# Kernel optimization log

Hardware: AMD Instinct MI355X
Metric: run time of the kernel (lower is better)

Reference implementation:

```python
import jax, jax.numpy as jnp
import numpy as np

TAU = 2.0
V_TH = 0.5
BN_EPS = 1e-5
ALPHA = 2.0  # spikingjelly surrogate.ATan default

@jax.custom_vjp
def spike_fn(x):
    # Heaviside forward, ATan surrogate backward (defined for fwdbwd parity)
    return (x >= 0.0).astype(x.dtype)

def _spike_fwd(x):
    return spike_fn(x), x

def _spike_bwd(x, g):
    return (g * (ALPHA / 2.0) / (1.0 + (jnp.pi / 2.0 * ALPHA * x) ** 2),)

spike_fn.defvjp(_spike_fwd, _spike_bwd)

def lif_multistep(x_seq):
    # MultiStepLIFNode: v <- v + (x - v)/tau ; spike = H(v - v_th) ; hard reset v<-v*(1-sg(spike))
    def step(v, x_t):
        v = v + (x_t - v) / TAU
        s = spike_fn(v - V_TH)
        v = v * (1.0 - jax.lax.stop_gradient(s))  # detach_reset=True, v_reset=0
        return v, s
    v0 = jnp.zeros_like(x_seq[0])
    _, spikes = jax.lax.scan(step, v0, x_seq)
    return spikes

def setup_inputs() -> dict:
    key = jax.random.key(0)
    k1, k2, k3 = jax.random.split(key, 3)
    T, B, N, D = 4, 64, 256, 512
    x = jax.random.normal(k1, (T, B, N, D), jnp.float32)
    mx = jax.random.normal(k2, (N, B, T, D), jnp.float32)
    W = jax.random.normal(k3, (D, D), jnp.float32) / np.sqrt(D).astype(np.float32)
    gamma = jnp.ones((D,), jnp.float32)
    beta = jnp.zeros((D,), jnp.float32)
    return {"x": x, "mx": mx, "W": W, "gamma": gamma, "beta": beta}

def reference(x, mx, W, gamma, beta):
    # mx: [N,B,T,D] -> transpose(0,2) -> [T,B,N,D]
    mxt = jnp.transpose(mx, (2, 1, 0, 3))
    # Linear (no bias): [T,B,N,D] @ W^T
    h = jnp.einsum('tbnd,ed->tbne', mxt, W)
    # BatchNorm1d(D) in training mode: stats over (T*B, N) per channel D (biased var)
    mean = h.mean(axis=(0, 1, 2))
    var = h.var(axis=(0, 1, 2))
    hn = (h - mean) * jax.lax.rsqrt(var + BN_EPS) * gamma + beta
    # LIF recurrence over T
    s = lif_multistep(hn)  # [T,B,N,D] binary spikes
    return x * s
```

## Files before the change

kernel.cpp:

```cpp
#include <hip/hip_runtime.h>
#include <math.h>

namespace {
constexpr int TDIM = 4, BDIM = 64, NDIM = 256, DDIM = 512;
constexpr int MROWS = 65536;
constexpr long long BND = 8388608LL;
constexpr double BN_EPS = 1e-5;

constexpr int BM = 64, BNT = 128, BK = 32;
constexpr int APITCH = BK + 2;
constexpr int WPITCH = BNT + 4;
constexpr int LDS_BYTES = (BM * APITCH + BK * WPITCH) * 8;

constexpr int BM3 = 128, BN3 = 64, BK3 = 16;
constexpr int AP3 = BM3 + 1;
constexpr int WP3 = BN3 + 1;

constexpr int NSA = 6, NSW = 5;
constexpr long long APL = 33554432LL;
constexpr long long WPL = 262144LL;
constexpr int LDSA8 = NSA * 64 * 64;
constexpr int LDSW8 = NSW * 64 * 64;
}

typedef double d4 __attribute__((ext_vector_type(4)));
typedef int i32x4 __attribute__((ext_vector_type(4)));
typedef int i32x16 __attribute__((ext_vector_type(16)));

__global__ void probe_k(double* __restrict__ rowmap)
{
    const int l = threadIdx.x;
    d4 z = {0.0, 0.0, 0.0, 0.0};
    d4 dr = __builtin_amdgcn_mfma_f64_16x16x4f64((double)(l & 15), 1.0, z, 0, 0, 0);
#pragma unroll
    for (int r = 0; r < 4; ++r)
        rowmap[l * 4 + r] = dr[r] * 0.25;
}

__global__ void probe8_k(double* __restrict__ irow8, double* __restrict__ icol8)
{
    const int l = threadIdx.x;
    i32x16 z;
#pragma unroll
    for (int r = 0; r < 16; ++r) z[r] = 0;
    const int mb = (l & 31) * 0x01010101;
    const int ob = 0x01010101;
    i32x4 am = {mb, mb, mb, mb};
    i32x4 a1 = {ob, ob, ob, ob};
    i32x16 d1 = __builtin_amdgcn_mfma_i32_32x32x32_i8(am, a1, z, 0, 0, 0);
#pragma unroll
    for (int r = 0; r < 16; ++r)
        irow8[l * 16 + r] = (double)d1[r] / 32.0;
    i32x16 d2 = __builtin_amdgcn_mfma_i32_32x32x32_i8(a1, am, z, 0, 0, 0);
    icol8[l] = (double)d2[0] / 32.0;
}

template<int NS>
__global__ __launch_bounds__(256)
void slice_k(const float* __restrict__ src, char* __restrict__ dst,
             long long n, long long plane, double F)
{
    const long long base = ((long long)blockIdx.x * 256 + threadIdx.x) * 8;
    if (base >= n) return;
    const float4 v0 = *(const float4*)(src + base);
    const float4 v1 = *(const float4*)(src + base + 4);
    const float vv[8] = {v0.x, v0.y, v0.z, v0.w, v1.x, v1.y, v1.z, v1.w};
    unsigned long long pk[NS];
#pragma unroll
    for (int s = 0; s < NS; ++s) pk[s] = 0ULL;
#pragma unroll
    for (int e = 0; e < 8; ++e) {
        double V = (double)vv[e] * F;
        double u = rint(V);
        double r = V - u;
        pk[0] |= ((unsigned long long)(unsigned char)(signed char)(int)u) << (8 * e);
#pragma unroll
        for (int s = 1; s < NS; ++s) {
            r *= 128.0;
            u = rint(r);
            r -= u;
            pk[s] |= ((unsigned long long)(unsigned char)(signed char)(int)u) << (8 * e);
        }
    }
#pragma unroll
    for (int s = 0; s < NS; ++s)
        *(unsigned long long*)(dst + s * plane + base) = pk[s];
}

__global__ __launch_bounds__(256, 2)
void gemm8_k(const char* __restrict__ Asl, const char* __restrict__ Wsl,
             double* __restrict__ hbuf, double* __restrict__ sums,
             const double* __restrict__ irow8, const double* __restrict__ icol8)
{
    __shared__ __align__(16) char sm8[LDSA8 + LDSW8];

    const int tid = threadIdx.x;
    const int bid = blockIdx.x;
    const int rb  = ((bid >> 6) << 3) | (bid & 7);
    const int cb  = (bid >> 3) & 7;
    const int row0 = rb * 64;
    const int col0 = cb * 64;

    const int w  = tid >> 6;
    const int l  = tid & 63;
    const int wr = w >> 1;
    const int wc = w & 1;

    const int sr = tid >> 2;
    const int sk = (tid & 3) * 16;
    const long long aoff = (long long)(row0 + sr) * DDIM + sk;
    const long long woff = (long long)(col0 + sr) * DDIM + sk;

    i32x16 acc[7];
#pragma unroll
    for (int g = 0; g < 7; ++g)
#pragma unroll
        for (int r = 0; r < 16; ++r) acc[g][r] = 0;

    i32x4 pfa[NSA], pfw[NSW];
#pragma unroll
    for (int s = 0; s < NSA; ++s)
        pfa[s] = *(const i32x4*)(Asl + s * APL + aoff);
#pragma unroll
    for (int s = 0; s < NSW; ++s)
        pfw[s] = *(const i32x4*)(Wsl + s * WPL + woff);

    const int swzS = (sr & 7) << 4;
    const int swzL = (l & 7) << 4;

    for (int c = 0; c < 8; ++c) {
        __syncthreads();
#pragma unroll
        for (int s = 0; s < NSA; ++s)
            *(i32x4*)(sm8 + ((s * 4096 + sr * 64 + sk) ^ swzS)) = pfa[s];
#pragma unroll
        for (int s = 0; s < NSW; ++s)
            *(i32x4*)(sm8 + LDSA8 + ((s * 4096 + sr * 64 + sk) ^ swzS)) = pfw[s];
        __syncthreads();

        if (c < 7) {
#pragma unroll
            for (int s = 0; s < NSA; ++s)
                pfa[s] = *(const i32x4*)(Asl + s * APL + aoff + (c + 1) * 64);
#pragma unroll
            for (int s = 0; s < NSW; ++s)
                pfw[s] = *(const i32x4*)(Wsl + s * WPL + woff + (c + 1) * 64);
        }

        const int arowB = (32 * wr + (l & 31)) * 64 + ((l >> 5) * 16);
        const int wrowB = (32 * wc + (l & 31)) * 64 + ((l >> 5) * 16);
#pragma unroll
        for (int h = 0; h < 2; ++h) {
            i32x4 af[NSA], wf[NSW];
#pragma unroll
            for (int s = 0; s < NSA; ++s)
                af[s] = *(const i32x4*)(sm8 + ((s * 4096 + arowB + h * 32) ^ swzL));
#pragma unroll
            for (int s = 0; s < NSW; ++s)
                wf[s] = *(const i32x4*)(sm8 + LDSA8 + ((s * 4096 + wrowB + h * 32) ^ swzL));
#pragma unroll
            for (int s = 0; s < NSA; ++s)
#pragma unroll
                for (int t = 0; t < NSW; ++t)
                    if (s + t <= 6)
                        acc[s + t] = __builtin_amdgcn_mfma_i32_32x32x32_i8(
                                         af[s], wf[t], acc[s + t], 0, 0, 0);
        }
    }

    int irw[16];
#pragma unroll
    for (int r = 0; r < 16; ++r) irw[r] = (int)irow8[l * 16 + r];
    const int icl = (int)icol8[l];

    const double C7 = 1.0 / 128.0, CMB = 1.0 / 1024.0;
    double lsum = 0.0, lsq = 0.0;
    const int colg = col0 + 32 * wc + icl;
#pragma unroll
    for (int r = 0; r < 16; ++r) {
        double t = (double)acc[6][r];
        t = fma(t, C7, (double)acc[5][r]);
        t = fma(t, C7, (double)acc[4][r]);
        t = fma(t, C7, (double)acc[3][r]);
        t = fma(t, C7, (double)acc[2][r]);
        t = fma(t, C7, (double)acc[1][r]);
        t = fma(t, C7, (double)acc[0][r]);
        const double h = t * CMB;
        const int rowg = row0 + 32 * wr + irw[r];
        hbuf[(size_t)rowg * DDIM + colg] = h;
        lsum += h;
        lsq = fma(h, h, lsq);
    }

    __syncthreads();
    double* Ss = (double*)sm8;
    const int ctr = wr * 2 + (l >> 5);
    const int cloc = 32 * wc + icl;
    Ss[cloc * 4 + ctr] = lsum;
    Ss[256 + cloc * 4 + ctr] = lsq;
    __syncthreads();
    if (tid < 64) {
        double s = 0.0, q = 0.0;
#pragma unroll
        for (int k = 0; k < 4; ++k) {
            s += Ss[tid * 4 + k];
            q += Ss[256 + tid * 4 + k];
        }
        atomicAdd(&sums[col0 + tid], s);
        atomicAdd(&sums[512 + col0 + tid], q);
    }
}

__global__ __launch_bounds__(256, 2)
void gemm3_k(const float* __restrict__ mx, const float* __restrict__ Wm,
             double* __restrict__ hbuf, double* __restrict__ sums,
             const double* __restrict__ rowmap)
{
    __shared__ double Atr[BK3 * AP3];
    __shared__ double Wt [BK3 * WP3];

    const int tid = threadIdx.x;
    const int bid = blockIdx.x;
    const int rb  = ((bid >> 6) << 3) | (bid & 7);
    const int cb  = (bid >> 3) & 7;
    const int row0 = rb * BM3;
    const int col0 = cb * BN3;

    const int w  = tid >> 6;
    const int l  = tid & 63;
    const int wr = w >> 1;
    const int wc = w & 1;
    const int lr = l & 15;
    const int kq = l >> 4;

    int irow[4];
#pragma unroll
    for (int r = 0; r < 4; ++r)
        irow[r] = (int)rowmap[l * 4 + r];

    const int arow = tid >> 1;
    const int af   = (tid & 1) * 8;
    const int wrow = tid >> 2;
    const int wf   = (tid & 3) * 4;
    const float* aSrc = mx + (size_t)(row0 + arow) * DDIM + af;
    const float* wSrc = Wm + (size_t)(col0 + wrow) * DDIM + wf;

    d4 acc[4][2];
#pragma unroll
    for (int i = 0; i < 4; ++i)
#pragma unroll
        for (int j = 0; j < 2; ++j) acc[i][j] = (d4){0.0, 0.0, 0.0, 0.0};

    float4 pa0 = *(const float4*)(aSrc + 0);
    float4 pa1 = *(const float4*)(aSrc + 4);
    float4 pw  = *(const float4*)(wSrc + 0);

    for (int kk = 0; kk < DDIM; kk += BK3) {
        __syncthreads();
        Atr[(af + 0) * AP3 + arow] = (double)pa0.x;
        Atr[(af + 1) * AP3 + arow] = (double)pa0.y;
        Atr[(af + 2) * AP3 + arow] = (double)pa0.z;
        Atr[(af + 3) * AP3 + arow] = (double)pa0.w;
        Atr[(af + 4) * AP3 + arow] = (double)pa1.x;
        Atr[(af + 5) * AP3 + arow] = (double)pa1.y;
        Atr[(af + 6) * AP3 + arow] = (double)pa1.z;
        Atr[(af + 7) * AP3 + arow] = (double)pa1.w;
        Wt[(wf + 0) * WP3 + wrow] = (double)pw.x;
        Wt[(wf + 1) * WP3 + wrow] = (double)pw.y;
        Wt[(wf + 2) * WP3 + wrow] = (double)pw.z;
        Wt[(wf + 3) * WP3 + wrow] = (double)pw.w;
        __syncthreads();

        if (kk + BK3 < DDIM) {
            pa0 = *(const float4*)(aSrc + kk + BK3 + 0);
            pa1 = *(const float4*)(aSrc + kk + BK3 + 4);
            pw  = *(const float4*)(wSrc + kk + BK3 + 0);
        }

#pragma unroll
        for (int ks = 0; ks < BK3 / 4; ++ks) {
            const int kabs = ks * 4 + kq;
            double a[4], b[2];
#pragma unroll
            for (int i = 0; i < 4; ++i)
                a[i] = Atr[kabs * AP3 + 64 * wr + 16 * i + lr];
#pragma unroll
            for (int j = 0; j < 2; ++j)
                b[j] = Wt[kabs * WP3 + 32 * wc + 16 * j + lr];
#pragma unroll
            for (int i = 0; i < 4; ++i)
#pragma unroll
                for (int j = 0; j < 2; ++j)
                    acc[i][j] = __builtin_amdgcn_mfma_f64_16x16x4f64(
                                    a[i], b[j], acc[i][j], 0, 0, 0);
        }
    }

#pragma unroll
    for (int i = 0; i < 4; ++i) {
#pragma unroll
        for (int j = 0; j < 2; ++j) {
            const size_t cbase = (size_t)col0 + 32 * wc + 16 * j + lr;
            const size_t rbase = (size_t)row0 + 64 * wr + 16 * i;
#pragma unroll
            for (int r = 0; r < 4; ++r)
                hbuf[(rbase + irow[r]) * DDIM + cbase] = acc[i][j][r];
        }
    }

    __syncthreads();
    double* Ssum = Atr;
    double* Ssq  = Atr + 512;
    const int ctr = wr * 4 + kq;
#pragma unroll
    for (int j = 0; j < 2; ++j) {
        const int cloc = 32 * wc + 16 * j + lr;
        double s = 0.0, q = 0.0;
#pragma unroll
        for (int i = 0; i < 4; ++i)
#pragma unroll
            for (int r = 0; r < 4; ++r) {
                const double v = acc[i][j][r];
                s += v;
                q = fma(v, v, q);
            }
        Ssum[cloc * 8 + ctr] = s;
        Ssq [cloc * 8 + ctr] = q;
    }
    __syncthreads();
    if (tid < 64) {
        double s = 0.0, q = 0.0;
#pragma unroll
        for (int c = 0; c < 8; ++c) {
            s += Ssum[tid * 8 + c];
            q += Ssq [tid * 8 + c];
        }
        atomicAdd(&sums[col0 + tid], s);
        atomicAdd(&sums[512 + col0 + tid], q);
    }
}

template<int MODE>
__global__ __launch_bounds__(256)
void gemm_k(const float* __restrict__ mx, const float* __restrict__ Wm,
            double* __restrict__ hbuf, double* __restrict__ sums,
            const double* __restrict__ scale, const double* __restrict__ shiftv,
            const float* __restrict__ x, float* __restrict__ out)
{
    __shared__ __align__(16) char smem[LDS_BYTES];
    double (*Ald)[APITCH] = reinterpret_cast<double(*)[APITCH]>(smem);
    double (*Wld)[WPITCH] = reinterpret_cast<double(*)[WPITCH]>(smem + (size_t)BM * APITCH * 8);

    const int tid  = threadIdx.x;
    const int rb   = blockIdx.x >> 2;
    const int cb   = blockIdx.x & 3;
    const int row0 = rb * BM;
    const int col0 = cb * BNT;

    const int arow = tid >> 2;
    const int ak   = (tid & 3) * 8;
    const int erow = tid >> 1;
    const int wk   = (tid & 1) * 16;

    const float* aSrc = mx + (size_t)(row0 + arow) * DDIM;
    const float* wSrc = Wm + (size_t)(col0 + erow) * DDIM;

    const int rg = tid >> 4;
    const int cg = tid & 15;

    double acc[4][8];
#pragma unroll
    for (int i = 0; i < 4; ++i)
#pragma unroll
        for (int j = 0; j < 8; ++j) acc[i][j] = 0.0;

    for (int kk = 0; kk < DDIM; kk += BK) {
        const float4 a0 = *(const float4*)(aSrc + kk + ak);
        const float4 a1 = *(const float4*)(aSrc + kk + ak + 4);
        const float4 w0 = *(const float4*)(wSrc + kk + wk);
        const float4 w1 = *(const float4*)(wSrc + kk + wk + 4);
        const float4 w2 = *(const float4*)(wSrc + kk + wk + 8);
        const float4 w3 = *(const float4*)(wSrc + kk + wk + 12);
        __syncthreads();
        Ald[arow][ak + 0] = (double)a0.x; Ald[arow][ak + 1] = (double)a0.y;
        Ald[arow][ak + 2] = (double)a0.z; Ald[arow][ak + 3] = (double)a0.w;
        Ald[arow][ak + 4] = (double)a1.x; Ald[arow][ak + 5] = (double)a1.y;
        Ald[arow][ak + 6] = (double)a1.z; Ald[arow][ak + 7] = (double)a1.w;
        const float wfv[16] = {w0.x, w0.y, w0.z, w0.w, w1.x, w1.y, w1.z, w1.w,
                               w2.x, w2.y, w2.z, w2.w, w3.x, w3.y, w3.z, w3.w};
#pragma unroll
        for (int q = 0; q < 16; ++q) Wld[wk + q][erow] = (double)wfv[q];
        __syncthreads();

#pragma unroll 4
        for (int d = 0; d < BK; ++d) {
            double a[4], wv[8];
#pragma unroll
            for (int i = 0; i < 4; ++i) a[i] = Ald[rg * 4 + i][d];
#pragma unroll
            for (int j = 0; j < 8; ++j) wv[j] = Wld[d][cg * 8 + j];
#pragma unroll
            for (int i = 0; i < 4; ++i)
#pragma unroll
                for (int j = 0; j < 8; ++j)
                    acc[i][j] = fma(a[i], wv[j], acc[i][j]);
        }
    }

    if (MODE <= 1) {
        __syncthreads();
        double* scr = reinterpret_cast<double*>(smem);
#pragma unroll
        for (int j = 0; j < 8; ++j) {
            const double s = acc[0][j] + acc[1][j] + acc[2][j] + acc[3][j];
            const double q = acc[0][j]*acc[0][j] + acc[1][j]*acc[1][j]
                           + acc[2][j]*acc[2][j] + acc[3][j]*acc[3][j];
            scr[(cg * 8 + j) * 16 + rg] = s;
            scr[2048 + (cg * 8 + j) * 16 + rg] = q;
        }
        __syncthreads();
        if (tid < 128) {
            double s = 0.0, q = 0.0;
#pragma unroll
            for (int r = 0; r < 16; ++r) {
                s += scr[tid * 16 + r];
                q += scr[2048 + tid * 16 + r];
            }
            atomicAdd(&sums[col0 + tid], s);
            atomicAdd(&sums[512 + col0 + tid], q);
        }
    }

    if (MODE == 2) {
        const int p  = rb * 16 + rg;
        const int nn = p >> 6;
        const int bb = p & 63;
#pragma unroll
        for (int j = 0; j < 8; ++j) {
            const int e = col0 + cg * 8 + j;
            const double sc = scale[e];
            const double sh = shiftv[e];
            const size_t basex = (size_t)bb * (NDIM * DDIM) + (size_t)nn * DDIM + e;
            double v = 0.0;
#pragma unroll
            for (int t = 0; t < 4; ++t) {
                const double hn = fma(acc[t][j], sc, sh);
                v = v + (hn - v) / 2.0;
                const bool s = (v - 0.5) >= 0.0;
                const size_t xi = (size_t)t * BND + basex;
                out[xi] = s ? x[xi] : 0.0f;
                if (s) v = 0.0;
            }
        }
    }
}

__global__ void zero_k(double* sums)
{
    const int i = blockIdx.x * 256 + threadIdx.x;
    if (i < 1024) sums[i] = 0.0;
}

__global__ void stat_k(const double* __restrict__ sums,
                       const float* __restrict__ gamma, const float* __restrict__ beta,
                       double* __restrict__ scale, double* __restrict__ shiftv)
{
    const int e = blockIdx.x * 256 + threadIdx.x;
    if (e < 512) {
        const double mean = sums[e] * (1.0 / 65536.0);
        const double msq  = sums[512 + e] * (1.0 / 65536.0);
        const double var  = msq - mean * mean;
        const double inv  = 1.0 / sqrt(var + BN_EPS);
        const double g    = (double)gamma[e] * inv;
        scale[e]  = g;
        shiftv[e] = (double)beta[e] - mean * g;
    }
}

__global__ __launch_bounds__(256)
void lifh_k(const double* __restrict__ hbuf, const double* __restrict__ scale,
            const double* __restrict__ shiftv, const float* __restrict__ x,
            float* __restrict__ out)
{
    const size_t i = (size_t)blockIdx.x * 256 + threadIdx.x;
    const int e  = (int)(i & 511);
    const size_t p = i >> 9;
    const int nn = (int)(p >> 6);
    const int bb = (int)(p & 63);
    const double sc = scale[e];
    const double sh = shiftv[e];
    const double* hp = hbuf + p * 2048 + e;
    const size_t basex = (size_t)bb * (NDIM * DDIM) + (size_t)nn * DDIM + e;
    double v = 0.0;
#pragma unroll
    for (int t = 0; t < 4; ++t) {
        const double hn = fma(hp[(size_t)t * 512], sc, sh);
        v = v + (hn - v) / 2.0;
        const bool s = (v - 0.5) >= 0.0;
        const size_t xi = (size_t)t * BND + basex;
        out[xi] = s ? x[xi] : 0.0f;
        if (s) v = 0.0;
    }
}

extern "C" void kernel_launch(void* const* d_in, const int* in_sizes, int n_in,
                              void* d_out, int out_size, void* d_ws, size_t ws_size,
                              hipStream_t stream)
{
    const float* x     = (const float*)d_in[0];
    const float* mx    = (const float*)d_in[1];
    const float* Wm    = (const float*)d_in[2];
    const float* gamma = (const float*)d_in[3];
    const float* beta  = (const float*)d_in[4];
    float* out = (float*)d_out;

    char* ws = (char*)d_ws;
    double* sums   = (double*)ws;
    double* scale  = (double*)(ws + 8192);
    double* shiftv = scale + 512;
    double* rowmap = (double*)(ws + 16384);
    double* irow8  = (double*)(ws + 18432);
    double* icol8  = (double*)(ws + 26624);
    double* hbuf   = (double*)(ws + 32768);

    const size_t HBSZ   = (size_t)MROWS * DDIM * 8;
    const size_t OFF_AS = 32768 + HBSZ;
    const size_t ASSZ   = (size_t)NSA * APL;
    const size_t OFF_WS = OFF_AS + ASSZ;
    const size_t WSSZ   = (size_t)NSW * WPL;
    const size_t need8  = OFF_WS + WSSZ;
    const size_t need_h = 32768 + HBSZ;

    hipLaunchKernelGGL(zero_k, dim3(4), dim3(256), 0, stream, sums);

    if (ws_size >= need8) {
        char* Asl = ws + OFF_AS;
        char* Wsl = ws + OFF_WS;
        hipLaunchKernelGGL(probe8_k, dim3(1), dim3(64), 0, stream, irow8, icol8);
        hipLaunchKernelGGL((slice_k<NSA>), dim3(16384), dim3(256), 0, stream,
                           mx, Asl, APL, APL, 4.0);
        hipLaunchKernelGGL((slice_k<NSW>), dim3(128), dim3(256), 0, stream,
                           Wm, Wsl, WPL, WPL, 256.0);
        hipLaunchKernelGGL(gemm8_k, dim3(8192), dim3(256), 0, stream,
                           Asl, Wsl, hbuf, sums, irow8, icol8);
        hipLaunchKernelGGL(stat_k, dim3(2), dim3(256), 0, stream,
                           sums, gamma, beta, scale, shiftv);
        hipLaunchKernelGGL(lifh_k, dim3(32768), dim3(256), 0, stream,
                           hbuf, scale, shiftv, x, out);
    } else if (ws_size >= need_h) {
        hipLaunchKernelGGL(probe_k, dim3(1), dim3(64), 0, stream, rowmap);
        hipLaunchKernelGGL(gemm3_k, dim3(4096), dim3(256), 0, stream,
                           mx, Wm, hbuf, sums, rowmap);
        hipLaunchKernelGGL(stat_k, dim3(2), dim3(256), 0, stream,
                           sums, gamma, beta, scale, shiftv);
        hipLaunchKernelGGL(lifh_k, dim3(32768), dim3(256), 0, stream,
                           hbuf, scale, shiftv, x, out);
    } else {
        hipLaunchKernelGGL((gemm_k<0>), dim3(4096), dim3(256), 0, stream,
                           mx, Wm, nullptr, sums, nullptr, nullptr, nullptr, nullptr);
        hipLaunchKernelGGL(stat_k, dim3(2), dim3(256), 0, stream,
                           sums, gamma, beta, scale, shiftv);
        hipLaunchKernelGGL((gemm_k<2>), dim3(4096), dim3(256), 0, stream,
                           mx, Wm, nullptr, nullptr, scale, shiftv, x, out);
    }
}
```

Measured before the change: 557.5 us.

## Tile-major int8 slice layout with direct global-to-LDS double-buffered loads

```diff
diff --git a/kernel.cpp b/kernel.cpp
--- a/kernel.cpp
+++ b/kernel.cpp
@@ -19,13 +19,16 @@
 constexpr int NSA = 6, NSW = 5;
 constexpr long long APL = 33554432LL;
 constexpr long long WPL = 262144LL;
-constexpr int LDSA8 = NSA * 64 * 64;
-constexpr int LDSW8 = NSW * 64 * 64;
+constexpr int CH8 = 22528;
 }
 
 typedef double d4 __attribute__((ext_vector_type(4)));
 typedef int i32x4 __attribute__((ext_vector_type(4)));
 typedef int i32x16 __attribute__((ext_vector_type(16)));
+
+#define GLOAD16(g, d) __builtin_amdgcn_global_load_lds( \
+    (const __attribute__((address_space(1))) void*)(g), \
+    (__attribute__((address_space(3))) void*)(d), 16, 0, 0)
 
 __global__ void probe_k(double* __restrict__ rowmap)
 {
@@ -55,117 +58,141 @@
     icol8[l] = (double)d2[0] / 32.0;
 }
 
-template<int NS>
 __global__ __launch_bounds__(256)
-void slice_k(const float* __restrict__ src, char* __restrict__ dst,
-             long long n, long long plane, double F)
-{
-    const long long base = ((long long)blockIdx.x * 256 + threadIdx.x) * 8;
-    if (base >= n) return;
-    const float4 v0 = *(const float4*)(src + base);
-    const float4 v1 = *(const float4*)(src + base + 4);
-    const float vv[8] = {v0.x, v0.y, v0.z, v0.w, v1.x, v1.y, v1.z, v1.w};
-    unsigned long long pk[NS];
-#pragma unroll
-    for (int s = 0; s < NS; ++s) pk[s] = 0ULL;
-#pragma unroll
-    for (int e = 0; e < 8; ++e) {
-        double V = (double)vv[e] * F;
+void slice_a_k(const float* __restrict__ src, char* __restrict__ dst)
+{
+    const int ri  = threadIdx.x & 63;
+    const int ks0 = threadIdx.x >> 6;
+    const long long row = (long long)blockIdx.x * 64 + ri;
+#pragma unroll 1
+    for (int it = 0; it < 8; ++it) {
+        const int kseg = it * 4 + ks0;
+        const float* sp = src + row * DDIM + kseg * 16;
+        union { char c[16]; i32x4 v; } pk[NSA];
+#pragma unroll
+        for (int e = 0; e < 16; ++e) {
+            double V = (double)sp[e] * 4.0;
+            double u = rint(V);
+            double r = V - u;
+            pk[0].c[e] = (char)(int)u;
+#pragma unroll
+            for (int s = 1; s < NSA; ++s) {
+                r *= 128.0;
+                u = rint(r);
+                r -= u;
+                pk[s].c[e] = (char)(int)u;
+            }
+        }
+        const long long base = (long long)blockIdx.x * 32768 + kseg * 1024 + ri * 16;
+#pragma unroll
+        for (int s = 0; s < NSA; ++s)
+            *(i32x4*)(dst + (long long)s * APL + base) = pk[s].v;
+    }
+}
+
+__global__ __launch_bounds__(256)
+void slice_w_k(const float* __restrict__ src, char* __restrict__ dst)
+{
+    const int cbk  = blockIdx.x >> 3;
+    const int kgrp = blockIdx.x & 7;
+    const int ci   = threadIdx.x & 63;
+    const int kseg = kgrp * 4 + (threadIdx.x >> 6);
+    const float* sp = src + (long long)(cbk * 64 + ci) * DDIM + kseg * 16;
+    union { char c[16]; i32x4 v; } pk[NSW];
+#pragma unroll
+    for (int e = 0; e < 16; ++e) {
+        double V = (double)sp[e] * 256.0;
         double u = rint(V);
         double r = V - u;
-        pk[0] |= ((unsigned long long)(unsigned char)(signed char)(int)u) << (8 * e);
-#pragma unroll
-        for (int s = 1; s < NS; ++s) {
+        pk[0].c[e] = (char)(int)u;
+#pragma unroll
+        for (int s = 1; s < NSW; ++s) {
             r *= 128.0;
             u = rint(r);
             r -= u;
-            pk[s] |= ((unsigned long long)(unsigned char)(signed char)(int)u) << (8 * e);
-        }
-    }
-#pragma unroll
-    for (int s = 0; s < NS; ++s)
-        *(unsigned long long*)(dst + s * plane + base) = pk[s];
-}
-
-__global__ __launch_bounds__(256, 2)
+            pk[s].c[e] = (char)(int)u;
+        }
+    }
+    const long long base = (long long)cbk * 32768 + kseg * 1024 + ci * 16;
+#pragma unroll
+    for (int s = 0; s < NSW; ++s)
+        *(i32x4*)(dst + (long long)s * WPL + base) = pk[s].v;
+}
+
+__device__ __forceinline__ void stage8(const char* Asl, const char* Wsl,
+                                       char* buf, long long aTile, long long wTile,
+                                       int c, int w, int l)
+{
+    char* bufA = buf;
+    char* bufW = buf + NSA * 2048;
+    for (int idx = w; idx < 22; idx += 4) {
+        if (idx < 12) {
+            const int s = idx >> 1, j = idx & 1;
+            const char* g = Asl + (long long)s * APL + aTile
+                          + (long long)(2 * c + j) * 1024 + l * 16;
+            GLOAD16(g, bufA + s * 2048 + j * 1024);
+        } else {
+            const int e = idx - 12, t = e >> 1, j = e & 1;
+            const char* g = Wsl + (long long)t * WPL + wTile
+                          + (long long)(2 * c + j) * 1024 + l * 16;
+            GLOAD16(g, bufW + t * 2048 + j * 1024);
+        }
+    }
+}
+
+__global__ __launch_bounds__(256, 3)
 void gemm8_k(const char* __restrict__ Asl, const char* __restrict__ Wsl,
              double* __restrict__ hbuf, double* __restrict__ sums,
              const double* __restrict__ irow8, const double* __restrict__ icol8)
 {
-    __shared__ __align__(16) char sm8[LDSA8 + LDSW8];
+    __shared__ __align__(16) char sm[2][CH8];
 
     const int tid = threadIdx.x;
     const int bid = blockIdx.x;
     const int rb  = ((bid >> 6) << 3) | (bid & 7);
     const int cb  = (bid >> 3) & 7;
-    const int row0 = rb * 64;
-    const int col0 = cb * 64;
 
     const int w  = tid >> 6;
     const int l  = tid & 63;
     const int wr = w >> 1;
     const int wc = w & 1;
 
-    const int sr = tid >> 2;
-    const int sk = (tid & 3) * 16;
-    const long long aoff = (long long)(row0 + sr) * DDIM + sk;
-    const long long woff = (long long)(col0 + sr) * DDIM + sk;
-
-    i32x16 acc[7];
-#pragma unroll
-    for (int g = 0; g < 7; ++g)
+    const long long aTile = (long long)rb * 32768;
+    const long long wTile = (long long)cb * 32768;
+
+    i32x16 acc[6];
+#pragma unroll
+    for (int g = 0; g < 6; ++g)
 #pragma unroll
         for (int r = 0; r < 16; ++r) acc[g][r] = 0;
 
-    i32x4 pfa[NSA], pfw[NSW];
-#pragma unroll
-    for (int s = 0; s < NSA; ++s)
-        pfa[s] = *(const i32x4*)(Asl + s * APL + aoff);
-#pragma unroll
-    for (int s = 0; s < NSW; ++s)
-        pfw[s] = *(const i32x4*)(Wsl + s * WPL + woff);
-
-    const int swzS = (sr & 7) << 4;
-    const int swzL = (l & 7) << 4;
-
-    for (int c = 0; c < 8; ++c) {
-        __syncthreads();
+    const int roA = (l >> 5) * 1024 + (32 * wr + (l & 31)) * 16;
+    const int roW = (l >> 5) * 1024 + (32 * wc + (l & 31)) * 16;
+
+    stage8(Asl, Wsl, sm[0], aTile, wTile, 0, w, l);
+    __syncthreads();
+
+    for (int c = 0; c < 16; ++c) {
+        if (c < 15)
+            stage8(Asl, Wsl, sm[(c + 1) & 1], aTile, wTile, c + 1, w, l);
+
+        const char* bA = sm[c & 1];
+        const char* bW = sm[c & 1] + NSA * 2048;
+        i32x4 af[NSA], wf[NSW];
 #pragma unroll
         for (int s = 0; s < NSA; ++s)
-            *(i32x4*)(sm8 + ((s * 4096 + sr * 64 + sk) ^ swzS)) = pfa[s];
-#pragma unroll
-        for (int s = 0; s < NSW; ++s)
-            *(i32x4*)(sm8 + LDSA8 + ((s * 4096 + sr * 64 + sk) ^ swzS)) = pfw[s];
-        __syncthreads();
-
-        if (c < 7) {
-#pragma unroll
-            for (int s = 0; s < NSA; ++s)
-                pfa[s] = *(const i32x4*)(Asl + s * APL + aoff + (c + 1) * 64);
-#pragma unroll
-            for (int s = 0; s < NSW; ++s)
-                pfw[s] = *(const i32x4*)(Wsl + s * WPL + woff + (c + 1) * 64);
-        }
-
-        const int arowB = (32 * wr + (l & 31)) * 64 + ((l >> 5) * 16);
-        const int wrowB = (32 * wc + (l & 31)) * 64 + ((l >> 5) * 16);
-#pragma unroll
-        for (int h = 0; h < 2; ++h) {
-            i32x4 af[NSA], wf[NSW];
-#pragma unroll
-            for (int s = 0; s < NSA; ++s)
-                af[s] = *(const i32x4*)(sm8 + ((s * 4096 + arowB + h * 32) ^ swzL));
-#pragma unroll
-            for (int s = 0; s < NSW; ++s)
-                wf[s] = *(const i32x4*)(sm8 + LDSA8 + ((s * 4096 + wrowB + h * 32) ^ swzL));
-#pragma unroll
-            for (int s = 0; s < NSA; ++s)
-#pragma unroll
-                for (int t = 0; t < NSW; ++t)
-                    if (s + t <= 6)
-                        acc[s + t] = __builtin_amdgcn_mfma_i32_32x32x32_i8(
-                                         af[s], wf[t], acc[s + t], 0, 0, 0);
-        }
+            af[s] = *(const i32x4*)(bA + s * 2048 + roA);
+#pragma unroll
+        for (int t = 0; t < NSW; ++t)
+            wf[t] = *(const i32x4*)(bW + t * 2048 + roW);
+#pragma unroll
+        for (int s = 0; s < NSA; ++s)
+#pragma unroll
+            for (int t = 0; t < NSW; ++t)
+                if (s + t <= 5)
+                    acc[s + t] = __builtin_amdgcn_mfma_i32_32x32x32_i8(
+                                     af[s], wf[t], acc[s + t], 0, 0, 0);
+        __syncthreads();
     }
 
     int irw[16];
@@ -175,25 +202,24 @@
 
     const double C7 = 1.0 / 128.0, CMB = 1.0 / 1024.0;
     double lsum = 0.0, lsq = 0.0;
-    const int colg = col0 + 32 * wc + icl;
+    const int colg = cb * 64 + 32 * wc + icl;
+    const int row0 = rb * 64 + 32 * wr;
 #pragma unroll
     for (int r = 0; r < 16; ++r) {
-        double t = (double)acc[6][r];
-        t = fma(t, C7, (double)acc[5][r]);
+        double t = (double)acc[5][r];
         t = fma(t, C7, (double)acc[4][r]);
         t = fma(t, C7, (double)acc[3][r]);
         t = fma(t, C7, (double)acc[2][r]);
         t = fma(t, C7, (double)acc[1][r]);
         t = fma(t, C7, (double)acc[0][r]);
         const double h = t * CMB;
-        const int rowg = row0 + 32 * wr + irw[r];
-        hbuf[(size_t)rowg * DDIM + colg] = h;
+        hbuf[(size_t)(row0 + irw[r]) * DDIM + colg] = h;
         lsum += h;
         lsq = fma(h, h, lsq);
     }
 
     __syncthreads();
-    double* Ss = (double*)sm8;
+    double* Ss = (double*)sm;
     const int ctr = wr * 2 + (l >> 5);
     const int cloc = 32 * wc + icl;
     Ss[cloc * 4 + ctr] = lsum;
@@ -206,8 +232,8 @@
             s += Ss[tid * 4 + k];
             q += Ss[256 + tid * 4 + k];
         }
-        atomicAdd(&sums[col0 + tid], s);
-        atomicAdd(&sums[512 + col0 + tid], q);
+        atomicAdd(&sums[cb * 64 + tid], s);
+        atomicAdd(&sums[512 + cb * 64 + tid], q);
     }
 }
 
@@ -537,10 +563,8 @@
         char* Asl = ws + OFF_AS;
         char* Wsl = ws + OFF_WS;
         hipLaunchKernelGGL(probe8_k, dim3(1), dim3(64), 0, stream, irow8, icol8);
-        hipLaunchKernelGGL((slice_k<NSA>), dim3(16384), dim3(256), 0, stream,
-                           mx, Asl, APL, APL, 4.0);
-        hipLaunchKernelGGL((slice_k<NSW>), dim3(128), dim3(256), 0, stream,
-                           Wm, Wsl, WPL, WPL, 256.0);
+        hipLaunchKernelGGL(slice_a_k, dim3(1024), dim3(256), 0, stream, mx, Asl);
+        hipLaunchKernelGGL(slice_w_k, dim3(64), dim3(256), 0, stream, Wm, Wsl);
         hipLaunchKernelGGL(gemm8_k, dim3(8192), dim3(256), 0, stream,
                            Asl, Wsl, hbuf, sums, irow8, icol8);
         hipLaunchKernelGGL(stat_k, dim3(2), dim3(256), 0, stream,
```

New measurement: 514.6 us. 1.08x faster.
